# Performance work log

Hardware: AMD Instinct MI355X
Metric: run time of the kernel (lower is better)

Reference implementation:

```python
import jax, jax.numpy as jnp
import numpy as np

B, D = 32, 512
N_IMG, N_KN = 50000, 8192
C = 32          # num_classes
R = 16          # image_retrieval_number
K = 8           # knowledge_retrieval_number
NEG = -1e9


def setup_inputs() -> dict:
    key = jax.random.key(0)
    k1, k2, k3, k4, k5 = jax.random.split(key, 5)
    return {
        'query_embeddings': jax.random.normal(k1, (B, D), dtype=jnp.float32),
        'all_image_embeddings': jax.random.normal(k2, (N_IMG, D), dtype=jnp.float32),
        'all_knowledge_embeddings': jax.random.normal(k3, (N_KN, D), dtype=jnp.float32),
        'image_labels': jax.random.randint(k4, (N_IMG,), 0, C, dtype=jnp.int32),
        'knowledge_labels': jax.random.randint(k5, (N_KN,), 0, C, dtype=jnp.int32),
    }


def reference(query_embeddings, all_image_embeddings, all_knowledge_embeddings,
              image_labels, knowledge_labels):
    classes = jnp.arange(C, dtype=jnp.int32)
    img_class_mask = image_labels[None, :] == classes[:, None]       # [C, N_img]
    kn_class_mask = knowledge_labels[None, :] == classes[:, None]    # [C, N_kn]

    # per-class masked similarity retrieval of images
    sims = query_embeddings @ all_image_embeddings.T                 # [B, N_img]
    masked = jnp.where(img_class_mask[None], sims[:, None, :], NEG)  # [B, C, N_img]
    img_vals, img_idx = jax.lax.top_k(masked, R)                     # [B, C, R]
    img_w = jax.nn.softmax(img_vals, axis=-1)
    similar_images = all_image_embeddings[img_idx]                   # [B, C, R, D]

    # image fusion (average of query and attention-weighted retrieved context)
    fused_img = jnp.einsum('bcr,bcrd->bcd', img_w, similar_images)
    enhanced_images = 0.5 * (query_embeddings[:, None, :] + fused_img)  # [B, C, D]

    # class-masked knowledge retrieval for every retrieved image
    ksims = jnp.einsum('bcrd,nd->bcrn', similar_images, all_knowledge_embeddings)
    kmasked = jnp.where(kn_class_mask[None, :, None, :], ksims, NEG)  # [B, C, R, N_kn]
    k_vals, k_idx = jax.lax.top_k(kmasked, K)                         # [B, C, R, K]
    k_w = jax.nn.softmax(k_vals, axis=-1)
    selected_knowledge = all_knowledge_embeddings[k_idx]              # [B, C, R, K, D]

    # knowledge fusion: weight over K, then over R with image weights, average w/ query
    fused_k = jnp.einsum('bcrk,bcrkd->bcrd', k_w, selected_knowledge)
    fused_k = jnp.einsum('bcr,bcrd->bcd', img_w, fused_k)
    enhanced_knowledge = 0.5 * (query_embeddings[:, None, :] + fused_k)  # [B, C, D]

    return enhanced_images, enhanced_knowledge
```

## Files before the change

kernel.cpp:

```cpp
#include <hip/hip_runtime.h>
#include <math.h>

#define NIMG 50000
#define NKN  8192
#define BB   32
#define DD   512
#define CC   32
#define RR   16
#define KK   8
#define MMAX 384
#define SPLIT 4
#define SD4  (DD / 4 / SPLIT)

typedef float f4v __attribute__((ext_vector_type(4)));

__global__ __launch_bounds__(256) void build_lists(const int* __restrict__ labels,
                                                   int n, int* __restrict__ cnt,
                                                   int* __restrict__ list, int stride) {
    int i = blockIdx.x * 256 + threadIdx.x;
    if (i < n) {
        int c = labels[i];
        int pos = atomicAdd(&cnt[c], 1);
        list[c * stride + pos] = i;
    }
}

__global__ __launch_bounds__(256, 2) void sims_kernel(const float* __restrict__ Q,
                                                      const float* __restrict__ I,
                                                      float* __restrict__ SP) {
    int slice = blockIdx.y, tid = threadIdx.x;
    __shared__ float4 qs[BB][SD4];
    for (int i = tid; i < BB * SD4; i += 256) {
        int b = i / SD4, d = i % SD4;
        qs[b][d] = ((const float4*)Q)[b * (DD / 4) + slice * SD4 + d];
    }
    __syncthreads();

    int n0 = blockIdx.x * 512 + tid;
    int n1 = n0 + 256;
    bool v1ok = n1 < NIMG;
    int n1c = v1ok ? n1 : 0;

    float a0[BB], a1[BB];
#pragma unroll
    for (int b = 0; b < BB; b++) { a0[b] = 0.f; a1[b] = 0.f; }

    const float4* r0 = (const float4*)(I + (size_t)n0 * DD) + slice * SD4;
    const float4* r1 = (const float4*)(I + (size_t)n1c * DD) + slice * SD4;
    for (int d = 0; d < SD4; d++) {
        float4 x0 = r0[d], x1 = r1[d];
#pragma unroll
        for (int b = 0; b < BB; b++) {
            float4 q = qs[b][d];
            a0[b] += x0.x * q.x + x0.y * q.y + x0.z * q.z + x0.w * q.w;
            a1[b] += x1.x * q.x + x1.y * q.y + x1.z * q.z + x1.w * q.w;
        }
    }
    float* out = SP + (size_t)slice * BB * NIMG;
#pragma unroll
    for (int b = 0; b < BB; b++) {
        out[(size_t)b * NIMG + n0] = a0[b];
        if (v1ok) out[(size_t)b * NIMG + n1] = a1[b];
    }
}

__global__ __launch_bounds__(256) void combine_s(float4* __restrict__ SP) {
    int i = blockIdx.x * 256 + threadIdx.x;
    const int n4 = BB * NIMG / 4;
    if (i >= n4) return;
    float4 s0 = SP[i], s1 = SP[i + n4], s2 = SP[i + 2 * n4], s3 = SP[i + 3 * n4];
    float4 r;
    r.x = ((s0.x + s1.x) + s2.x) + s3.x;
    r.y = ((s0.y + s1.y) + s2.y) + s3.y;
    r.z = ((s0.z + s1.z) + s2.z) + s3.z;
    r.w = ((s0.w + s1.w) + s2.w) + s3.w;
    SP[i] = r;
}

__global__ __launch_bounds__(256) void topk_img(const float* __restrict__ S,
                                                const int* __restrict__ cnt,
                                                const int* __restrict__ list,
                                                int* __restrict__ t_idx,
                                                float* __restrict__ t_w) {
    int c = blockIdx.x, b = blockIdx.y, tid = threadIdx.x;
    int wave = tid >> 6, lane = tid & 63;
    __shared__ float wv_s[4];
    __shared__ int   wi_s[4];
    __shared__ float kv_s[RR];
    __shared__ int   ki_s[RR];

    int m = cnt[c];
    const float* Sb = S + (size_t)b * NIMG;

    float cv0, cv1, cv2, cv3, cv4, cv5, cv6;
    int   ci0, ci1, ci2, ci3, ci4, ci5, ci6;
#define LOADC(t) { int j = tid + t * 256; \
        if (j < m) { int n = list[c * NIMG + j]; cv##t = Sb[n]; ci##t = n; } \
        else { cv##t = -1e30f; ci##t = 0x7fffffff; } }
    LOADC(0) LOADC(1) LOADC(2) LOADC(3) LOADC(4) LOADC(5) LOADC(6)
#undef LOADC

    unsigned used = 0;
#define CANDT(t) { if (!(used & (1u << t)) && \
                       (cv##t > mv || (cv##t == mv && ci##t < mj))) \
                   { mv = cv##t; mj = ci##t; mt = t; } }
#define RND(k) { \
        float mv = -1e30f; int mj = 0x7fffffff; int mt = -1; \
        CANDT(0) CANDT(1) CANDT(2) CANDT(3) CANDT(4) CANDT(5) CANDT(6) \
        int lmj = mj; \
        for (int off = 32; off > 0; off >>= 1) { \
            float ov = __shfl_xor(mv, off); \
            int   oj = __shfl_xor(mj, off); \
            if (ov > mv || (ov == mv && oj < mj)) { mv = ov; mj = oj; } \
        } \
        if (lane == 0) { wv_s[wave] = mv; wi_s[wave] = mj; } \
        __syncthreads(); \
        float gv = wv_s[0]; int gj = wi_s[0]; \
        if (wv_s[1] > gv || (wv_s[1] == gv && wi_s[1] < gj)) { gv = wv_s[1]; gj = wi_s[1]; } \
        if (wv_s[2] > gv || (wv_s[2] == gv && wi_s[2] < gj)) { gv = wv_s[2]; gj = wi_s[2]; } \
        if (wv_s[3] > gv || (wv_s[3] == gv && wi_s[3] < gj)) { gv = wv_s[3]; gj = wi_s[3]; } \
        if (mt >= 0 && lmj == gj && lmj != 0x7fffffff) used |= (1u << mt); \
        if (tid == 0) { kv_s[k] = gv; ki_s[k] = gj; } \
        __syncthreads(); }

    RND(0)  RND(1)  RND(2)  RND(3)  RND(4)  RND(5)  RND(6)  RND(7)
    RND(8)  RND(9)  RND(10) RND(11) RND(12) RND(13) RND(14) RND(15)
#undef RND
#undef CANDT

    if (tid == 0) {
        float mx = kv_s[0], s = 0.f, e[RR];
#pragma unroll
        for (int k = 0; k < RR; k++) { e[k] = expf(kv_s[k] - mx); s += e[k]; }
        float inv = 1.f / s;
        size_t o = ((size_t)(b * CC) + c) * RR;
#pragma unroll
        for (int k = 0; k < RR; k++) { t_w[o + k] = e[k] * inv; t_idx[o + k] = ki_s[k]; }
    }
}

__global__ __launch_bounds__(256) void img_kernel(const float* __restrict__ Q,
                                                  const float* __restrict__ I,
                                                  const int* __restrict__ t_idx,
                                                  const float* __restrict__ t_w,
                                                  float* __restrict__ out) {
    int c = blockIdx.x, b = blockIdx.y, tid = threadIdx.x;
    __shared__ float w[RR];
    __shared__ int   id[RR];
    if (tid < RR) {
        size_t o = ((size_t)(b * CC) + c) * RR;
        w[tid] = t_w[o + tid]; id[tid] = t_idx[o + tid];
    }
    __syncthreads();
    for (int d = tid; d < DD; d += 256) {
        float acc = 0.f;
#pragma unroll
        for (int r = 0; r < RR; r++) acc += w[r] * I[(size_t)id[r] * DD + d];
        out[((size_t)(b * CC) + c) * DD + d] = 0.5f * (Q[b * DD + d] + acc);
    }
}

__global__ __launch_bounds__(256) void transpose_kn(const float* __restrict__ KN,
                                                    const int* __restrict__ kcnt,
                                                    const int* __restrict__ klist,
                                                    float4* __restrict__ KT4) {
    int c = blockIdx.x;
    int w = threadIdx.x >> 6, lane = threadIdx.x & 63;
    int j = blockIdx.y * 4 + w;
    int m = kcnt[c]; if (m > MMAX) m = MMAX;
    int row = klist[c * NKN + (j < m ? j : 0)];
    const float4* src = (const float4*)(KN + (size_t)row * DD);
    float4* dst = KT4 + (size_t)c * (DD / 4) * MMAX;
    float4 v0 = src[lane], v1 = src[lane + 64];
    dst[(size_t)lane * MMAX + j]        = v0;
    dst[(size_t)(lane + 64) * MMAX + j] = v1;
}

__global__ __launch_bounds__(256, 4) void knowledge_kernel(const float* __restrict__ Q,
                                                           const float* __restrict__ I,
                                                           const float* __restrict__ KN,
                                                           const float4* __restrict__ KT4,
                                                           const int* __restrict__ kcnt,
                                                           const int* __restrict__ klist,
                                                           const int* __restrict__ t_idx,
                                                           const float* __restrict__ t_w,
                                                           float* __restrict__ outk) {
    int c = blockIdx.x, b = blockIdx.y;
    int tid = threadIdx.x, wave = tid >> 6, lane = tid & 63;
    int rbase = wave * 4;

    __shared__ float4 simg[RR][DD / 4];
    __shared__ float  s_iw[RR];
    __shared__ int    s_ii[RR];
    __shared__ float  wgt[RR][KK];
    __shared__ int    kidx[RR][KK];

    if (tid < RR) {
        size_t o = ((size_t)(b * CC) + c) * RR;
        s_iw[tid] = t_w[o + tid]; s_ii[tid] = t_idx[o + tid];
    }
    __syncthreads();

    for (int i = tid; i < RR * DD / 4; i += 256) {
        int r = i >> 7, d4 = i & 127;
        simg[r][d4] = ((const float4*)(I + (size_t)s_ii[r] * DD))[d4];
    }

    int m = kcnt[c]; if (m > MMAX) m = MMAX;
    int ng = (m + 63) >> 6;
    const float4* KTc = KT4 + (size_t)c * (DD / 4) * MMAX;

    f4v A0 = 0.f, A1 = 0.f, A2 = 0.f, A3 = 0.f, A4 = 0.f, A5 = 0.f;

    __syncthreads();

#define LG(g) float4 kk##g = p[g * 64];
#define FG(g, rr) A##g[rr] = fmaf(kk##g.x, u.x, fmaf(kk##g.y, u.y, \
                   fmaf(kk##g.z, u.z, fmaf(kk##g.w, u.w, A##g[rr]))));
#define RRBLK(rr, FMAS) { float4 u = simg[rbase + rr][d4]; FMAS }
#define SCORE(LOADS, F0, F1, F2, F3) \
        for (int d4 = 0; d4 < DD / 4; d4++) { \
            const float4* p = KTc + (size_t)d4 * MMAX + lane; \
            LOADS \
            RRBLK(0, F0) RRBLK(1, F1) RRBLK(2, F2) RRBLK(3, F3) }

    if (ng <= 4) {
        SCORE(LG(0) LG(1) LG(2) LG(3),
              FG(0,0) FG(1,0) FG(2,0) FG(3,0),
              FG(0,1) FG(1,1) FG(2,1) FG(3,1),
              FG(0,2) FG(1,2) FG(2,2) FG(3,2),
              FG(0,3) FG(1,3) FG(2,3) FG(3,3))
    } else if (ng == 5) {
        SCORE(LG(0) LG(1) LG(2) LG(3) LG(4),
              FG(0,0) FG(1,0) FG(2,0) FG(3,0) FG(4,0),
              FG(0,1) FG(1,1) FG(2,1) FG(3,1) FG(4,1),
              FG(0,2) FG(1,2) FG(2,2) FG(3,2) FG(4,2),
              FG(0,3) FG(1,3) FG(2,3) FG(3,3) FG(4,3))
    } else {
        SCORE(LG(0) LG(1) LG(2) LG(3) LG(4) LG(5),
              FG(0,0) FG(1,0) FG(2,0) FG(3,0) FG(4,0) FG(5,0),
              FG(0,1) FG(1,1) FG(2,1) FG(3,1) FG(4,1) FG(5,1),
              FG(0,2) FG(1,2) FG(2,2) FG(3,2) FG(4,2) FG(5,2),
              FG(0,3) FG(1,3) FG(2,3) FG(3,3) FG(4,3) FG(5,3))
    }
#undef SCORE
#undef RRBLK
#undef FG
#undef LG

#define CAND(t) { if (!(used & (1u << t)) && \
                      (lv##t > mv || (lv##t == mv && (t * 64 + lane) < mj))) \
                  { mv = lv##t; mj = t * 64 + lane; mt = t; } }

#define ROUND(k) { \
        float mv = -1e30f; int mj = 0x7fffffff; int mt = -1; \
        CAND(0) CAND(1) CAND(2) CAND(3) CAND(4) CAND(5) \
        int cj = mj; \
        for (int off = 32; off > 0; off >>= 1) { \
            float ov = __shfl_xor(mv, off); \
            int   oj = __shfl_xor(mj, off); \
            if (ov > mv || (ov == mv && oj < mj)) { mv = ov; mj = oj; } \
        } \
        if (cj == mj && mt >= 0) used |= (1u << mt); \
        if (lane == k) myj = mj; \
        kv##k = mv; }

#define TOPK_RR(rr) { \
        int r = rbase + rr; \
        float lv0 = (0 * 64 + lane < m) ? A0[rr] : -1e30f; \
        float lv1 = (1 * 64 + lane < m) ? A1[rr] : -1e30f; \
        float lv2 = (2 * 64 + lane < m) ? A2[rr] : -1e30f; \
        float lv3 = (3 * 64 + lane < m) ? A3[rr] : -1e30f; \
        float lv4 = (4 * 64 + lane < m) ? A4[rr] : -1e30f; \
        float lv5 = (5 * 64 + lane < m) ? A5[rr] : -1e30f; \
        unsigned used = 0; int myj = 0; \
        float kv0, kv1, kv2, kv3, kv4, kv5, kv6, kv7; \
        ROUND(0) ROUND(1) ROUND(2) ROUND(3) \
        ROUND(4) ROUND(5) ROUND(6) ROUND(7) \
        if (lane < KK) kidx[r][lane] = klist[c * NKN + myj]; \
        if (lane == 0) { \
            float e0 = 1.f; \
            float e1 = expf(kv1 - kv0), e2 = expf(kv2 - kv0), e3 = expf(kv3 - kv0); \
            float e4 = expf(kv4 - kv0), e5 = expf(kv5 - kv0), e6 = expf(kv6 - kv0); \
            float e7 = expf(kv7 - kv0); \
            float s = e0 + e1 + e2 + e3 + e4 + e5 + e6 + e7; \
            float wr = s_iw[r] / s; \
            wgt[r][0] = e0 * wr; wgt[r][1] = e1 * wr; wgt[r][2] = e2 * wr; \
            wgt[r][3] = e3 * wr; wgt[r][4] = e4 * wr; wgt[r][5] = e5 * wr; \
            wgt[r][6] = e6 * wr; wgt[r][7] = e7 * wr; \
        } }

    TOPK_RR(0) TOPK_RR(1) TOPK_RR(2) TOPK_RR(3)
#undef TOPK_RR
#undef ROUND
#undef CAND

    __syncthreads();

    float acc0 = 0.f, acc1 = 0.f;
#pragma unroll 8
    for (int p = 0; p < RR * KK; p++) {
        int r = p >> 3, k = p & 7;
        float w = wgt[r][k];
        const float* kp = KN + (size_t)kidx[r][k] * DD;
        acc0 += w * kp[tid];
        acc1 += w * kp[tid + 256];
    }
    size_t o = ((size_t)(b * CC) + c) * DD;
    outk[o + tid]       = 0.5f * (Q[b * DD + tid] + acc0);
    outk[o + tid + 256] = 0.5f * (Q[b * DD + tid + 256] + acc1);
}

extern "C" void kernel_launch(void* const* d_in, const int* in_sizes, int n_in,
                              void* d_out, int out_size, void* d_ws, size_t ws_size,
                              hipStream_t stream) {
    const float* Q  = (const float*)d_in[0];
    const float* I  = (const float*)d_in[1];
    const float* KN = (const float*)d_in[2];
    const int* ilab = (const int*)d_in[3];
    const int* klab = (const int*)d_in[4];

    char* ws = (char*)d_ws;
    float* SP       = (float*)ws;  ws += (size_t)SPLIT * BB * NIMG * 4;
    int*   img_list = (int*)ws;    ws += (size_t)CC * NIMG * 4;
    int*   kn_list  = (int*)ws;    ws += (size_t)CC * NKN * 4;
    int*   t_idx    = (int*)ws;    ws += (size_t)BB * CC * RR * 4;
    float* t_w      = (float*)ws;  ws += (size_t)BB * CC * RR * 4;
    int*   img_cnt  = (int*)ws;    ws += CC * 4;
    int*   kn_cnt   = (int*)ws;    ws += CC * 4;
    ws = (char*)(((size_t)ws + 255) & ~(size_t)255);
    float4* KT4     = (float4*)ws; ws += (size_t)CC * (DD / 4) * MMAX * 16;

    float* out_img = (float*)d_out;
    float* out_kn  = out_img + (size_t)BB * CC * DD;

    hipMemsetAsync(img_cnt, 0, 2 * CC * 4, stream);

    build_lists<<<(NIMG + 255) / 256, 256, 0, stream>>>(ilab, NIMG, img_cnt, img_list, NIMG);
    build_lists<<<(NKN  + 255) / 256, 256, 0, stream>>>(klab, NKN,  kn_cnt,  kn_list,  NKN);
    transpose_kn<<<dim3(CC, MMAX / 4), 256, 0, stream>>>(KN, kn_cnt, kn_list, KT4);
    sims_kernel<<<dim3((NIMG + 511) / 512, SPLIT), 256, 0, stream>>>(Q, I, SP);
    combine_s<<<(BB * NIMG / 4 + 255) / 256, 256, 0, stream>>>((float4*)SP);
    topk_img<<<dim3(CC, BB), 256, 0, stream>>>(SP, img_cnt, img_list, t_idx, t_w);
    img_kernel<<<dim3(CC, BB), 256, 0, stream>>>(Q, I, t_idx, t_w, (float*)d_out);
    knowledge_kernel<<<dim3(CC, BB), 256, 0, stream>>>(Q, I, KN, KT4, kn_cnt, kn_list, t_idx, t_w, out_kn);
}
```

Baseline: 366.6 us.

## Double the sims split-K, software-pipeline knowledge loads, alias KT4 onto SP

The image similarity GEMM is split 8 ways along D instead of 4, giving more blocks for parallelism, and the combine kernel now sums 8 partial slabs. The knowledge scoring loop for the 4- and 5-group cases is restructured to double-buffer the KT4 global loads one d4 step ahead of the FMAs, hiding load latency. KT4 now reuses the SP workspace, so transpose_kn is moved after topk_img, which shrinks the workspace footprint. In exchange, combine reads twice as much partial data and the prefetch raises register pressure.

```diff
diff --git a/kernel.cpp b/kernel.cpp
--- a/kernel.cpp
+++ b/kernel.cpp
@@ -9,7 +9,7 @@
 #define RR   16
 #define KK   8
 #define MMAX 384
-#define SPLIT 4
+#define SPLIT 8
 #define SD4  (DD / 4 / SPLIT)
 
 typedef float f4v __attribute__((ext_vector_type(4)));
@@ -68,12 +68,14 @@
     int i = blockIdx.x * 256 + threadIdx.x;
     const int n4 = BB * NIMG / 4;
     if (i >= n4) return;
-    float4 s0 = SP[i], s1 = SP[i + n4], s2 = SP[i + 2 * n4], s3 = SP[i + 3 * n4];
+    float4 s0 = SP[i],          s1 = SP[i + n4],     s2 = SP[i + 2 * n4],
+           s3 = SP[i + 3 * n4], s4 = SP[i + 4 * n4], s5 = SP[i + 5 * n4],
+           s6 = SP[i + 6 * n4], s7 = SP[i + 7 * n4];
     float4 r;
-    r.x = ((s0.x + s1.x) + s2.x) + s3.x;
-    r.y = ((s0.y + s1.y) + s2.y) + s3.y;
-    r.z = ((s0.z + s1.z) + s2.z) + s3.z;
-    r.w = ((s0.w + s1.w) + s2.w) + s3.w;
+    r.x = ((((((s0.x + s1.x) + s2.x) + s3.x) + s4.x) + s5.x) + s6.x) + s7.x;
+    r.y = ((((((s0.y + s1.y) + s2.y) + s3.y) + s4.y) + s5.y) + s6.y) + s7.y;
+    r.z = ((((((s0.z + s1.z) + s2.z) + s3.z) + s4.z) + s5.z) + s6.z) + s7.z;
+    r.w = ((((((s0.w + s1.w) + s2.w) + s3.w) + s4.w) + s5.w) + s6.w) + s7.w;
     SP[i] = r;
 }
 
@@ -214,39 +216,62 @@
 
     __syncthreads();
 
-#define LG(g) float4 kk##g = p[g * 64];
-#define FG(g, rr) A##g[rr] = fmaf(kk##g.x, u.x, fmaf(kk##g.y, u.y, \
-                   fmaf(kk##g.z, u.z, fmaf(kk##g.w, u.w, A##g[rr]))));
-#define RRBLK(rr, FMAS) { float4 u = simg[rbase + rr][d4]; FMAS }
-#define SCORE(LOADS, F0, F1, F2, F3) \
-        for (int d4 = 0; d4 < DD / 4; d4++) { \
-            const float4* p = KTc + (size_t)d4 * MMAX + lane; \
-            LOADS \
-            RRBLK(0, F0) RRBLK(1, F1) RRBLK(2, F2) RRBLK(3, F3) }
+#define FG2(K, ACC, rr) ACC[rr] = fmaf(K.x, u.x, fmaf(K.y, u.y, \
+                         fmaf(K.z, u.z, fmaf(K.w, u.w, ACC[rr]))));
+
+#define PH4(K0, K1, K2, K3, D4) \
+    { float4 u = simg[rbase + 0][D4]; FG2(K0,A0,0) FG2(K1,A1,0) FG2(K2,A2,0) FG2(K3,A3,0) } \
+    { float4 u = simg[rbase + 1][D4]; FG2(K0,A0,1) FG2(K1,A1,1) FG2(K2,A2,1) FG2(K3,A3,1) } \
+    { float4 u = simg[rbase + 2][D4]; FG2(K0,A0,2) FG2(K1,A1,2) FG2(K2,A2,2) FG2(K3,A3,2) } \
+    { float4 u = simg[rbase + 3][D4]; FG2(K0,A0,3) FG2(K1,A1,3) FG2(K2,A2,3) FG2(K3,A3,3) }
+
+#define PH5(K0, K1, K2, K3, K4, D4) \
+    { float4 u = simg[rbase + 0][D4]; FG2(K0,A0,0) FG2(K1,A1,0) FG2(K2,A2,0) FG2(K3,A3,0) FG2(K4,A4,0) } \
+    { float4 u = simg[rbase + 1][D4]; FG2(K0,A0,1) FG2(K1,A1,1) FG2(K2,A2,1) FG2(K3,A3,1) FG2(K4,A4,1) } \
+    { float4 u = simg[rbase + 2][D4]; FG2(K0,A0,2) FG2(K1,A1,2) FG2(K2,A2,2) FG2(K3,A3,2) FG2(K4,A4,2) } \
+    { float4 u = simg[rbase + 3][D4]; FG2(K0,A0,3) FG2(K1,A1,3) FG2(K2,A2,3) FG2(K3,A3,3) FG2(K4,A4,3) }
+
+#define PH6(K0, K1, K2, K3, K4, K5, D4) \
+    { float4 u = simg[rbase + 0][D4]; FG2(K0,A0,0) FG2(K1,A1,0) FG2(K2,A2,0) FG2(K3,A3,0) FG2(K4,A4,0) FG2(K5,A5,0) } \
+    { float4 u = simg[rbase + 1][D4]; FG2(K0,A0,1) FG2(K1,A1,1) FG2(K2,A2,1) FG2(K3,A3,1) FG2(K4,A4,1) FG2(K5,A5,1) } \
+    { float4 u = simg[rbase + 2][D4]; FG2(K0,A0,2) FG2(K1,A1,2) FG2(K2,A2,2) FG2(K3,A3,2) FG2(K4,A4,2) FG2(K5,A5,2) } \
+    { float4 u = simg[rbase + 3][D4]; FG2(K0,A0,3) FG2(K1,A1,3) FG2(K2,A2,3) FG2(K3,A3,3) FG2(K4,A4,3) FG2(K5,A5,3) }
 
     if (ng <= 4) {
-        SCORE(LG(0) LG(1) LG(2) LG(3),
-              FG(0,0) FG(1,0) FG(2,0) FG(3,0),
-              FG(0,1) FG(1,1) FG(2,1) FG(3,1),
-              FG(0,2) FG(1,2) FG(2,2) FG(3,2),
-              FG(0,3) FG(1,3) FG(2,3) FG(3,3))
+        const float4* p0 = KTc + lane;
+        float4 xa0 = p0[0], xa1 = p0[64], xa2 = p0[128], xa3 = p0[192];
+        for (int d4 = 0; d4 < DD / 4; d4 += 2) {
+            const float4* pb = KTc + (size_t)(d4 + 1) * MMAX + lane;
+            float4 xb0 = pb[0], xb1 = pb[64], xb2 = pb[128], xb3 = pb[192];
+            PH4(xa0, xa1, xa2, xa3, d4)
+            int nx = (d4 + 2 < DD / 4) ? (d4 + 2) : (DD / 4 - 1);
+            const float4* pa = KTc + (size_t)nx * MMAX + lane;
+            xa0 = pa[0]; xa1 = pa[64]; xa2 = pa[128]; xa3 = pa[192];
+            PH4(xb0, xb1, xb2, xb3, d4 + 1)
+        }
     } else if (ng == 5) {
-        SCORE(LG(0) LG(1) LG(2) LG(3) LG(4),
-              FG(0,0) FG(1,0) FG(2,0) FG(3,0) FG(4,0),
-              FG(0,1) FG(1,1) FG(2,1) FG(3,1) FG(4,1),
-              FG(0,2) FG(1,2) FG(2,2) FG(3,2) FG(4,2),
-              FG(0,3) FG(1,3) FG(2,3) FG(3,3) FG(4,3))
+        const float4* p0 = KTc + lane;
+        float4 xa0 = p0[0], xa1 = p0[64], xa2 = p0[128], xa3 = p0[192], xa4 = p0[256];
+        for (int d4 = 0; d4 < DD / 4; d4 += 2) {
+            const float4* pb = KTc + (size_t)(d4 + 1) * MMAX + lane;
+            float4 xb0 = pb[0], xb1 = pb[64], xb2 = pb[128], xb3 = pb[192], xb4 = pb[256];
+            PH5(xa0, xa1, xa2, xa3, xa4, d4)
+            int nx = (d4 + 2 < DD / 4) ? (d4 + 2) : (DD / 4 - 1);
+            const float4* pa = KTc + (size_t)nx * MMAX + lane;
+            xa0 = pa[0]; xa1 = pa[64]; xa2 = pa[128]; xa3 = pa[192]; xa4 = pa[256];
+            PH5(xb0, xb1, xb2, xb3, xb4, d4 + 1)
+        }
     } else {
-        SCORE(LG(0) LG(1) LG(2) LG(3) LG(4) LG(5),
-              FG(0,0) FG(1,0) FG(2,0) FG(3,0) FG(4,0) FG(5,0),
-              FG(0,1) FG(1,1) FG(2,1) FG(3,1) FG(4,1) FG(5,1),
-              FG(0,2) FG(1,2) FG(2,2) FG(3,2) FG(4,2) FG(5,2),
-              FG(0,3) FG(1,3) FG(2,3) FG(3,3) FG(4,3) FG(5,3))
-    }
-#undef SCORE
-#undef RRBLK
-#undef FG
-#undef LG
+        for (int d4 = 0; d4 < DD / 4; d4++) {
+            const float4* p = KTc + (size_t)d4 * MMAX + lane;
+            float4 k0 = p[0], k1 = p[64], k2 = p[128], k3 = p[192], k4 = p[256], k5 = p[320];
+            PH6(k0, k1, k2, k3, k4, k5, d4)
+        }
+    }
+#undef PH6
+#undef PH5
+#undef PH4
+#undef FG2
 
 #define CAND(t) { if (!(used & (1u << t)) && \
                       (lv##t > mv || (lv##t == mv && (t * 64 + lane) < mj))) \
@@ -322,14 +347,13 @@
 
     char* ws = (char*)d_ws;
     float* SP       = (float*)ws;  ws += (size_t)SPLIT * BB * NIMG * 4;
+    float4* KT4     = (float4*)SP;
     int*   img_list = (int*)ws;    ws += (size_t)CC * NIMG * 4;
     int*   kn_list  = (int*)ws;    ws += (size_t)CC * NKN * 4;
     int*   t_idx    = (int*)ws;    ws += (size_t)BB * CC * RR * 4;
     float* t_w      = (float*)ws;  ws += (size_t)BB * CC * RR * 4;
     int*   img_cnt  = (int*)ws;    ws += CC * 4;
     int*   kn_cnt   = (int*)ws;    ws += CC * 4;
-    ws = (char*)(((size_t)ws + 255) & ~(size_t)255);
-    float4* KT4     = (float4*)ws; ws += (size_t)CC * (DD / 4) * MMAX * 16;
 
     float* out_img = (float*)d_out;
     float* out_kn  = out_img + (size_t)BB * CC * DD;
@@ -338,10 +362,10 @@
 
     build_lists<<<(NIMG + 255) / 256, 256, 0, stream>>>(ilab, NIMG, img_cnt, img_list, NIMG);
     build_lists<<<(NKN  + 255) / 256, 256, 0, stream>>>(klab, NKN,  kn_cnt,  kn_list,  NKN);
-    transpose_kn<<<dim3(CC, MMAX / 4), 256, 0, stream>>>(KN, kn_cnt, kn_list, KT4);
     sims_kernel<<<dim3((NIMG + 511) / 512, SPLIT), 256, 0, stream>>>(Q, I, SP);
     combine_s<<<(BB * NIMG / 4 + 255) / 256, 256, 0, stream>>>((float4*)SP);
     topk_img<<<dim3(CC, BB), 256, 0, stream>>>(SP, img_cnt, img_list, t_idx, t_w);
     img_kernel<<<dim3(CC, BB), 256, 0, stream>>>(Q, I, t_idx, t_w, (float*)d_out);
+    transpose_kn<<<dim3(CC, MMAX / 4), 256, 0, stream>>>(KN, kn_cnt, kn_list, KT4);
     knowledge_kernel<<<dim3(CC, BB), 256, 0, stream>>>(Q, I, KN, KT4, kn_cnt, kn_list, t_idx, t_w, out_kn);
 }
```

New measurement: 439.1 us. 1.2x slower.
